# Performance work log

Hardware: AMD Instinct MI355X
Metric: run time of the kernel (lower is better)

Reference implementation:

```python
import jax, jax.numpy as jnp
import numpy as np

HEADS = 8
DIM_HEAD = 64
SCALE = DIM_HEAD ** -0.5


def setup_inputs() -> dict:
    key = jax.random.key(0)
    ks = jax.random.split(key, 5)
    B, N, M, D = 8, 1024, 1024, 512
    inner = HEADS * DIM_HEAD  # 512
    return {
        "x": jax.random.normal(ks[0], (B, N, D), dtype=jnp.float32),
        "context": jax.random.normal(ks[1], (B, M, D), dtype=jnp.float32),
        "Wq": jax.random.normal(ks[2], (D, inner), dtype=jnp.float32) * (D ** -0.5),
        "Wkv": jax.random.normal(ks[3], (D, 2 * inner), dtype=jnp.float32) * (D ** -0.5),
        "Wo": jax.random.normal(ks[4], (inner, D), dtype=jnp.float32) * (inner ** -0.5),
        "bo": jnp.zeros((D,), dtype=jnp.float32),
    }


def reference(x, context, Wq, Wkv, Wo, bo):
    B, N, D = x.shape
    M = context.shape[1]
    q = x @ Wq                      # [B, N, inner]
    kv = context @ Wkv              # [B, M, 2*inner]
    k, v = jnp.split(kv, 2, axis=-1)
    # b n (h d) -> b h n d
    split_heads = lambda t: t.reshape(t.shape[0], t.shape[1], HEADS, DIM_HEAD).transpose(0, 2, 1, 3)
    q, k, v = split_heads(q), split_heads(k), split_heads(v)
    dots = jnp.einsum('bhid,bhjd->bhij', q, k) * SCALE  # [B, H, N, M]
    attn = jax.nn.softmax(dots, axis=-1)
    out = jnp.einsum('bhij,bhjd->bhid', attn, v)        # [B, H, N, d]
    out = out.transpose(0, 2, 1, 3).reshape(B, N, HEADS * DIM_HEAD)
    return out @ Wo + bo            # [B, N, D]
```

## Files before the change

### kernel.cpp

```cpp
#include <hip/hip_runtime.h>
#include <stdint.h>

#define LOG2E 1.44269504088896340736f
#define QSCALE (0.125f * LOG2E)

typedef __bf16 bf16x8 __attribute__((ext_vector_type(8)));
typedef float floatx4 __attribute__((ext_vector_type(4)));

__device__ __forceinline__ unsigned short bfbits(float f) {
  __bf16 h = (__bf16)f;
  return __builtin_bit_cast(unsigned short, h);
}

__device__ __forceinline__ float fast_exp2(float x) {
#if __has_builtin(__builtin_amdgcn_exp2f)
  return __builtin_amdgcn_exp2f(x);
#else
  return exp2f(x);
#endif
}

__device__ __forceinline__ void gl2lds16(const void* g, void* l) {
  __builtin_amdgcn_global_load_lds((const __attribute__((address_space(1))) void*)g,
                                   (__attribute__((address_space(3))) void*)l, 16, 0, 0);
}

__global__ __launch_bounds__(256)
void prep_kernel(const float* __restrict__ x, const float* __restrict__ ctx,
                 const float* __restrict__ Wq, const float* __restrict__ Wkv,
                 const float* __restrict__ Wo,
                 unsigned short* __restrict__ Xb, unsigned short* __restrict__ Cb,
                 unsigned short* __restrict__ WqT, unsigned short* __restrict__ WkvT,
                 unsigned short* __restrict__ WoT) {
  int blk = blockIdx.x;
  int tid = threadIdx.x;
  if (blk < 8192) {
    const float* in = blk < 4096 ? x : ctx;
    unsigned short* out = blk < 4096 ? Xb : Cb;
    int i = (((blk & 4095) * 256) + tid) * 4;
    float4 v = *(const float4*)(in + i);
    unsigned long long pk = (unsigned long long)bfbits(v.x)
                          | ((unsigned long long)bfbits(v.y) << 16)
                          | ((unsigned long long)bfbits(v.z) << 32)
                          | ((unsigned long long)bfbits(v.w) << 48);
    *(unsigned long long*)(out + i) = pk;
  } else {
    __shared__ float tile[32][33];
    int t = blk - 8192;
    const float* in; unsigned short* out; int N; int tb;
    if (t < 256)      { in = Wq;  out = WqT;  N = 512;  tb = t; }
    else if (t < 768) { in = Wkv; out = WkvT; N = 1024; tb = t - 256; }
    else              { in = Wo;  out = WoT;  N = 512;  tb = t - 768; }
    const int K = 512;
    int nbx = N / 32;
    int n0 = (tb % nbx) * 32, k0 = (tb / nbx) * 32;
    int tx = tid & 31, ty = tid >> 5;
#pragma unroll
    for (int r = ty; r < 32; r += 8)
      tile[r][tx] = in[(long)(k0 + r) * N + n0 + tx];
    __syncthreads();
#pragma unroll
    for (int r = ty; r < 32; r += 8)
      out[(long)(n0 + r) * K + k0 + tx] = bfbits(tile[tx][r]);
  }
}

__global__ __launch_bounds__(256)
void proj_gemm(const unsigned short* __restrict__ Xb, const unsigned short* __restrict__ Cb,
               const unsigned short* __restrict__ WqT, const unsigned short* __restrict__ WkvT,
               unsigned short* __restrict__ Qb, unsigned short* __restrict__ Kb,
               unsigned short* __restrict__ Vt) {
  __shared__ unsigned short As[128 * 32];
  __shared__ unsigned short Bs[128 * 32];

  int idx = blockIdx.x;
  const unsigned short* A; const unsigned short* Bt;
  long bm, bn; int role;
  if (idx < 256) { role = 0; A = Xb; Bt = WqT;  bn = (long)(idx & 3) * 128; bm = (long)(idx >> 2) * 128; }
  else { idx -= 256; role = 1; A = Cb; Bt = WkvT; bn = (long)(idx & 7) * 128; bm = (long)(idx >> 3) * 128; }

  const int tid = threadIdx.x;
  const int wave = tid >> 6;
  const int lane = tid & 63;
  const int l15 = lane & 15;
  const int q4 = lane >> 4;
  const int wm = (wave & 1) * 64;
  const int wn = (wave >> 1) * 64;
  const int K = 512;

  floatx4 acc[4][4];
#pragma unroll
  for (int i = 0; i < 4; ++i)
#pragma unroll
    for (int j = 0; j < 4; ++j) { acc[i][j][0]=0.f; acc[i][j][1]=0.f; acc[i][j][2]=0.f; acc[i][j][3]=0.f; }

  for (int k0 = 0; k0 < K; k0 += 32) {
#pragma unroll
    for (int cc = 0; cc < 2; ++cc) {
      int c = cc * 256 + tid;
      int r = c >> 2, kc = c & 3;
      gl2lds16(A + (bm + r) * (long)K + k0 + kc * 8, (char*)As + c * 16);
      gl2lds16(Bt + (bn + r) * (long)K + k0 + kc * 8, (char*)Bs + c * 16);
    }
    __syncthreads();
    bf16x8 af[4], bfr[4];
#pragma unroll
    for (int i = 0; i < 4; ++i)
      af[i] = *(const bf16x8*)(As + (wm + i * 16 + l15) * 32 + q4 * 8);
#pragma unroll
    for (int j = 0; j < 4; ++j)
      bfr[j] = *(const bf16x8*)(Bs + (wn + j * 16 + l15) * 32 + q4 * 8);
#pragma unroll
    for (int i = 0; i < 4; ++i)
#pragma unroll
      for (int j = 0; j < 4; ++j)
        acc[i][j] = __builtin_amdgcn_mfma_f32_16x16x32_bf16(af[i], bfr[j], acc[i][j], 0, 0, 0);
    __syncthreads();
  }

  const bool vrole = (role == 1) && (bn >= 512);
#pragma unroll
  for (int i = 0; i < 4; ++i) {
#pragma unroll
    for (int j = 0; j < 4; ++j) {
      long col = bn + wn + j * 16 + l15;
      if (vrole) {
        long h = (col - 512) >> 6, d = col & 63;
        long row0 = bm + wm + i * 16 + q4 * 4;
        long b = row0 >> 10, m0 = row0 & 1023;
        unsigned long long pk = (unsigned long long)bfbits(acc[i][j][0])
                              | ((unsigned long long)bfbits(acc[i][j][1]) << 16)
                              | ((unsigned long long)bfbits(acc[i][j][2]) << 32)
                              | ((unsigned long long)bfbits(acc[i][j][3]) << 48);
        *(unsigned long long*)(Vt + ((b * 8 + h) * 64 + d) * 1024 + m0) = pk;
      } else {
        long h = col >> 6, d = col & 63;
#pragma unroll
        for (int r = 0; r < 4; ++r) {
          long row = bm + wm + i * 16 + q4 * 4 + r;
          long b = row >> 10, n = row & 1023;
          float v = acc[i][j][r];
          if (role == 0) Qb[((b * 8 + h) * 1024 + n) * 64 + d] = bfbits(v * QSCALE);
          else           Kb[((b * 8 + h) * 1024 + n) * 64 + d] = bfbits(v);
        }
      }
    }
  }
}

__global__ __launch_bounds__(256)
void attn_kernel(const unsigned short* __restrict__ Qb,
                 const unsigned short* __restrict__ Kb,
                 const unsigned short* __restrict__ Vt,
                 unsigned short* __restrict__ Ob)
{
  __shared__ unsigned short Ksm[2][4096];
  __shared__ unsigned short Vsm[2][4096];
  __shared__ unsigned short Psm[64 * 64];

  const int tid = threadIdx.x;
  const int wave = tid >> 6;
  const int lane = tid & 63;
  const int l15 = lane & 15;
  const int q4 = lane >> 4;
  const int bh = blockIdx.x;
  const int nb = blockIdx.y;

  bf16x8 qf[2];
#pragma unroll
  for (int ks = 0; ks < 2; ++ks)
    qf[ks] = *(const bf16x8*)(Qb + ((long)bh * 1024 + nb * 64 + wave * 16 + l15) * 64 + ks * 32 + q4 * 8);

  floatx4 acc[4];
#pragma unroll
  for (int d = 0; d < 4; ++d) { acc[d][0]=0.f; acc[d][1]=0.f; acc[d][2]=0.f; acc[d][3]=0.f; }
  float suml = 0.0f;

  const unsigned short* Kbase = Kb + (long)bh * 65536;
  const unsigned short* Vbase = Vt + (long)bh * 65536;
  int koff[2], voff[2], lds16[2];
#pragma unroll
  for (int cc = 0; cc < 2; ++cc) {
    int c = cc * 256 + tid;
    int jrow = c >> 3;
    int cact = (c & 7) ^ (jrow & 7);
    koff[cc] = jrow * 64 + cact * 8;
    voff[cc] = jrow * 1024 + cact * 8;
    lds16[cc] = c * 16;
  }
#pragma unroll
  for (int cc = 0; cc < 2; ++cc) {
    gl2lds16(Kbase + koff[cc], (char*)Ksm[0] + lds16[cc]);
    gl2lds16(Vbase + voff[cc], (char*)Vsm[0] + lds16[cc]);
  }

  const int prow = wave * 16 + l15;

  for (int t = 0; t < 16; ++t) {
    __syncthreads();
    const int cur = t & 1;
    if (t + 1 < 16) {
      const int nxt = cur ^ 1;
#pragma unroll
      for (int cc = 0; cc < 2; ++cc) {
        gl2lds16(Kbase + (t + 1) * 4096 + koff[cc], (char*)Ksm[nxt] + lds16[cc]);
        gl2lds16(Vbase + (t + 1) * 64 + voff[cc], (char*)Vsm[nxt] + lds16[cc]);
      }
    }

    floatx4 st[4];
#pragma unroll
    for (int jn = 0; jn < 4; ++jn) { st[jn][0]=0.f; st[jn][1]=0.f; st[jn][2]=0.f; st[jn][3]=0.f; }
#pragma unroll
    for (int ks = 0; ks < 2; ++ks) {
      bf16x8 kfr[4];
#pragma unroll
      for (int jn = 0; jn < 4; ++jn) {
        int j = jn * 16 + l15;
        int cact = (ks * 4 + q4) ^ (j & 7);
        kfr[jn] = *(const bf16x8*)(Ksm[cur] + j * 64 + cact * 8);
      }
#pragma unroll
      for (int jn = 0; jn < 4; ++jn)
        st[jn] = __builtin_amdgcn_mfma_f32_16x16x32_bf16(kfr[jn], qf[ks], st[jn], 0, 0, 0);
    }

#pragma unroll
    for (int jn = 0; jn < 4; ++jn) {
      float p0 = fast_exp2(st[jn][0]);
      float p1 = fast_exp2(st[jn][1]);
      float p2 = fast_exp2(st[jn][2]);
      float p3 = fast_exp2(st[jn][3]);
      suml += (p0 + p1) + (p2 + p3);
      unsigned long long pk = (unsigned long long)bfbits(p0)
                            | ((unsigned long long)bfbits(p1) << 16)
                            | ((unsigned long long)bfbits(p2) << 32)
                            | ((unsigned long long)bfbits(p3) << 48);
      int ch8 = (jn * 2 + (q4 >> 1)) ^ (prow & 7);
      *(unsigned long long*)(Psm + prow * 64 + ch8 * 8 + (q4 & 1) * 4) = pk;
    }
    __asm__ volatile("s_waitcnt lgkmcnt(0)" ::: "memory");

#pragma unroll
    for (int ks = 0; ks < 2; ++ks) {
      bf16x8 pa = *(const bf16x8*)(Psm + prow * 64 + (((ks * 4 + q4) ^ (prow & 7)) * 8));
      bf16x8 vb[4];
#pragma unroll
      for (int dn = 0; dn < 4; ++dn) {
        int dd = dn * 16 + l15;
        int cact = (ks * 4 + q4) ^ (dd & 7);
        vb[dn] = *(const bf16x8*)(Vsm[cur] + dd * 64 + cact * 8);
      }
#pragma unroll
      for (int dn = 0; dn < 4; ++dn)
        acc[dn] = __builtin_amdgcn_mfma_f32_16x16x32_bf16(pa, vb[dn], acc[dn], 0, 0, 0);
    }
  }

  float l = suml;
  l += __shfl_xor(l, 16, 64);
  l += __shfl_xor(l, 32, 64);
  float inv = 1.0f / l;
  float invr[4];
#pragma unroll
  for (int r = 0; r < 4; ++r) invr[r] = __shfl(inv, q4 * 4 + r, 64);

  const int b = bh >> 3, h = bh & 7;
#pragma unroll
  for (int dn = 0; dn < 4; ++dn) {
#pragma unroll
    for (int r = 0; r < 4; ++r) {
      long row = (long)b * 1024 + nb * 64 + wave * 16 + q4 * 4 + r;
      long col = h * 64 + dn * 16 + l15;
      Ob[row * 512 + col] = bfbits(acc[dn][r] * invr[r]);
    }
  }
}

__global__ __launch_bounds__(256)
void out_gemm(const unsigned short* __restrict__ A,
              const unsigned short* __restrict__ Bt,
              float* __restrict__ outF, const float* __restrict__ bias) {
  __shared__ unsigned short As[64 * 32];
  __shared__ unsigned short Bs[128 * 32];

  const int tid = threadIdx.x;
  const int wave = tid >> 6;
  const int lane = tid & 63;
  const int l15 = lane & 15;
  const int q4 = lane >> 4;
  const int wm = (wave & 1) * 32;
  const int wn = (wave >> 1) * 64;
  const long bm = (long)blockIdx.y * 64;
  const long bn = (long)blockIdx.x * 128;
  const int K = 512, N = 512;

  floatx4 acc[2][4];
#pragma unroll
  for (int i = 0; i < 2; ++i)
#pragma unroll
    for (int j = 0; j < 4; ++j) { acc[i][j][0]=0.f; acc[i][j][1]=0.f; acc[i][j][2]=0.f; acc[i][j][3]=0.f; }

  for (int k0 = 0; k0 < K; k0 += 32) {
    {
      int r = tid >> 2, kc = tid & 3;
      gl2lds16(A + (bm + r) * (long)K + k0 + kc * 8, (char*)As + tid * 16);
    }
#pragma unroll
    for (int cc = 0; cc < 2; ++cc) {
      int c = cc * 256 + tid;
      int r = c >> 2, kc = c & 3;
      gl2lds16(Bt + (bn + r) * (long)K + k0 + kc * 8, (char*)Bs + c * 16);
    }
    __syncthreads();
    bf16x8 af[2], bfr[4];
#pragma unroll
    for (int i = 0; i < 2; ++i)
      af[i] = *(const bf16x8*)(As + (wm + i * 16 + l15) * 32 + q4 * 8);
#pragma unroll
    for (int j = 0; j < 4; ++j)
      bfr[j] = *(const bf16x8*)(Bs + (wn + j * 16 + l15) * 32 + q4 * 8);
#pragma unroll
    for (int i = 0; i < 2; ++i)
#pragma unroll
      for (int j = 0; j < 4; ++j)
        acc[i][j] = __builtin_amdgcn_mfma_f32_16x16x32_bf16(af[i], bfr[j], acc[i][j], 0, 0, 0);
    __syncthreads();
  }

#pragma unroll
  for (int i = 0; i < 2; ++i) {
#pragma unroll
    for (int j = 0; j < 4; ++j) {
      long col = bn + wn + j * 16 + l15;
      float bv = bias[col];
#pragma unroll
      for (int r = 0; r < 4; ++r) {
        long row = bm + wm + i * 16 + q4 * 4 + r;
        outF[row * (long)N + col] = acc[i][j][r] + bv;
      }
    }
  }
}

extern "C" void kernel_launch(void* const* d_in, const int* in_sizes, int n_in,
                              void* d_out, int out_size, void* d_ws, size_t ws_size,
                              hipStream_t stream) {
  const float* x   = (const float*)d_in[0];
  const float* ctx = (const float*)d_in[1];
  const float* Wq  = (const float*)d_in[2];
  const float* Wkv = (const float*)d_in[3];
  const float* Wo  = (const float*)d_in[4];
  const float* bo  = (const float*)d_in[5];
  float* out = (float*)d_out;

  char* ws = (char*)d_ws;
  unsigned short* Xb   = (unsigned short*)(ws);
  unsigned short* Cb   = (unsigned short*)(ws + (8u  << 20));
  unsigned short* WqT  = (unsigned short*)(ws + (16u << 20));
  unsigned short* WkvT = (unsigned short*)(ws + (17u << 20));
  unsigned short* WoT  = (unsigned short*)(ws + (19u << 20));
  unsigned short* Qb   = (unsigned short*)(ws + (20u << 20));
  unsigned short* Kb   = (unsigned short*)(ws + (28u << 20));
  unsigned short* Vt   = (unsigned short*)(ws + (36u << 20));
  unsigned short* Ob   = (unsigned short*)(ws + (44u << 20));

  prep_kernel<<<9216, 256, 0, stream>>>(x, ctx, Wq, Wkv, Wo, Xb, Cb, WqT, WkvT, WoT);
  proj_gemm<<<768, 256, 0, stream>>>(Xb, Cb, WqT, WkvT, Qb, Kb, Vt);
  attn_kernel<<<dim3(64, 16), 256, 0, stream>>>(Qb, Kb, Vt, Ob);
  out_gemm<<<dim3(4, 128), 256, 0, stream>>>(Ob, WoT, out, bo);
}
```

Measured before the change: 157.2 us.

## Double attention query tile per block to reuse K/V tiles across 128 rows

Each attention block now processes 128 query rows (32 per wave, two 16-row MFMA sub-tiles) instead of 64, halving the grid along the query dimension. Each K/V tile staged in shared memory is reused by twice as many queries, and K fragments loaded from LDS feed two MFMAs, so global and LDS traffic per unit of work drops. The cost is more registers and a larger P buffer in shared memory, which may lower occupancy, and only 512 blocks are launched.

```diff
diff --git a/kernel.cpp b/kernel.cpp
--- a/kernel.cpp
+++ b/kernel.cpp
@@ -156,7 +156,7 @@
 {
   __shared__ unsigned short Ksm[2][4096];
   __shared__ unsigned short Vsm[2][4096];
-  __shared__ unsigned short Psm[64 * 64];
+  __shared__ unsigned short Psm[128 * 64];
 
   const int tid = threadIdx.x;
   const int wave = tid >> 6;
@@ -166,15 +166,21 @@
   const int bh = blockIdx.x;
   const int nb = blockIdx.y;
 
-  bf16x8 qf[2];
-#pragma unroll
-  for (int ks = 0; ks < 2; ++ks)
-    qf[ks] = *(const bf16x8*)(Qb + ((long)bh * 1024 + nb * 64 + wave * 16 + l15) * 64 + ks * 32 + q4 * 8);
-
-  floatx4 acc[4];
-#pragma unroll
-  for (int d = 0; d < 4; ++d) { acc[d][0]=0.f; acc[d][1]=0.f; acc[d][2]=0.f; acc[d][3]=0.f; }
-  float suml = 0.0f;
+  const long qrow0 = (long)bh * 1024 + nb * 128 + wave * 32;
+
+  bf16x8 qf[2][2];
+#pragma unroll
+  for (int qn = 0; qn < 2; ++qn)
+#pragma unroll
+    for (int ks = 0; ks < 2; ++ks)
+      qf[qn][ks] = *(const bf16x8*)(Qb + (qrow0 + qn * 16 + l15) * 64 + ks * 32 + q4 * 8);
+
+  floatx4 acc[2][4];
+#pragma unroll
+  for (int i = 0; i < 2; ++i)
+#pragma unroll
+    for (int d = 0; d < 4; ++d) { acc[i][d][0]=0.f; acc[i][d][1]=0.f; acc[i][d][2]=0.f; acc[i][d][3]=0.f; }
+  float suml[2] = {0.0f, 0.0f};
 
   const unsigned short* Kbase = Kb + (long)bh * 65536;
   const unsigned short* Vbase = Vt + (long)bh * 65536;
@@ -194,8 +200,6 @@
     gl2lds16(Vbase + voff[cc], (char*)Vsm[0] + lds16[cc]);
   }
 
-  const int prow = wave * 16 + l15;
-
   for (int t = 0; t < 16; ++t) {
     __syncthreads();
     const int cur = t & 1;
@@ -208,9 +212,11 @@
       }
     }
 
-    floatx4 st[4];
-#pragma unroll
-    for (int jn = 0; jn < 4; ++jn) { st[jn][0]=0.f; st[jn][1]=0.f; st[jn][2]=0.f; st[jn][3]=0.f; }
+    floatx4 st[4][2];
+#pragma unroll
+    for (int jn = 0; jn < 4; ++jn)
+#pragma unroll
+      for (int qn = 0; qn < 2; ++qn) { st[jn][qn][0]=0.f; st[jn][qn][1]=0.f; st[jn][qn][2]=0.f; st[jn][qn][3]=0.f; }
 #pragma unroll
     for (int ks = 0; ks < 2; ++ks) {
       bf16x8 kfr[4];
@@ -222,29 +228,40 @@
       }
 #pragma unroll
       for (int jn = 0; jn < 4; ++jn)
-        st[jn] = __builtin_amdgcn_mfma_f32_16x16x32_bf16(kfr[jn], qf[ks], st[jn], 0, 0, 0);
-    }
-
-#pragma unroll
-    for (int jn = 0; jn < 4; ++jn) {
-      float p0 = fast_exp2(st[jn][0]);
-      float p1 = fast_exp2(st[jn][1]);
-      float p2 = fast_exp2(st[jn][2]);
-      float p3 = fast_exp2(st[jn][3]);
-      suml += (p0 + p1) + (p2 + p3);
-      unsigned long long pk = (unsigned long long)bfbits(p0)
-                            | ((unsigned long long)bfbits(p1) << 16)
-                            | ((unsigned long long)bfbits(p2) << 32)
-                            | ((unsigned long long)bfbits(p3) << 48);
-      int ch8 = (jn * 2 + (q4 >> 1)) ^ (prow & 7);
-      *(unsigned long long*)(Psm + prow * 64 + ch8 * 8 + (q4 & 1) * 4) = pk;
+#pragma unroll
+        for (int qn = 0; qn < 2; ++qn)
+          st[jn][qn] = __builtin_amdgcn_mfma_f32_16x16x32_bf16(kfr[jn], qf[qn][ks], st[jn][qn], 0, 0, 0);
+    }
+
+#pragma unroll
+    for (int qn = 0; qn < 2; ++qn) {
+      int prow = wave * 32 + qn * 16 + l15;
+#pragma unroll
+      for (int jn = 0; jn < 4; ++jn) {
+        float p0 = fast_exp2(st[jn][qn][0]);
+        float p1 = fast_exp2(st[jn][qn][1]);
+        float p2 = fast_exp2(st[jn][qn][2]);
+        float p3 = fast_exp2(st[jn][qn][3]);
+        suml[qn] += (p0 + p1) + (p2 + p3);
+        unsigned long long pk = (unsigned long long)bfbits(p0)
+                              | ((unsigned long long)bfbits(p1) << 16)
+                              | ((unsigned long long)bfbits(p2) << 32)
+                              | ((unsigned long long)bfbits(p3) << 48);
+        int ch16 = (jn * 2 + (q4 >> 1)) ^ (prow & 7);
+        *(unsigned long long*)(Psm + prow * 64 + ch16 * 8 + (q4 & 1) * 4) = pk;
+      }
     }
     __asm__ volatile("s_waitcnt lgkmcnt(0)" ::: "memory");
 
 #pragma unroll
     for (int ks = 0; ks < 2; ++ks) {
-      bf16x8 pa = *(const bf16x8*)(Psm + prow * 64 + (((ks * 4 + q4) ^ (prow & 7)) * 8));
-      bf16x8 vb[4];
+      bf16x8 pa[2], vb[4];
+#pragma unroll
+      for (int i = 0; i < 2; ++i) {
+        int m = wave * 32 + i * 16 + l15;
+        int cact = (ks * 4 + q4) ^ (m & 7);
+        pa[i] = *(const bf16x8*)(Psm + m * 64 + cact * 8);
+      }
 #pragma unroll
       for (int dn = 0; dn < 4; ++dn) {
         int dd = dn * 16 + l15;
@@ -252,27 +269,35 @@
         vb[dn] = *(const bf16x8*)(Vsm[cur] + dd * 64 + cact * 8);
       }
 #pragma unroll
-      for (int dn = 0; dn < 4; ++dn)
-        acc[dn] = __builtin_amdgcn_mfma_f32_16x16x32_bf16(pa, vb[dn], acc[dn], 0, 0, 0);
-    }
-  }
-
-  float l = suml;
-  l += __shfl_xor(l, 16, 64);
-  l += __shfl_xor(l, 32, 64);
-  float inv = 1.0f / l;
-  float invr[4];
-#pragma unroll
-  for (int r = 0; r < 4; ++r) invr[r] = __shfl(inv, q4 * 4 + r, 64);
+      for (int i = 0; i < 2; ++i)
+#pragma unroll
+        for (int dn = 0; dn < 4; ++dn)
+          acc[i][dn] = __builtin_amdgcn_mfma_f32_16x16x32_bf16(pa[i], vb[dn], acc[i][dn], 0, 0, 0);
+    }
+  }
+
+  float inv[2], invr[2][4];
+#pragma unroll
+  for (int qn = 0; qn < 2; ++qn) {
+    float l = suml[qn];
+    l += __shfl_xor(l, 16, 64);
+    l += __shfl_xor(l, 32, 64);
+    inv[qn] = 1.0f / l;
+#pragma unroll
+    for (int r = 0; r < 4; ++r) invr[qn][r] = __shfl(inv[qn], q4 * 4 + r, 64);
+  }
 
   const int b = bh >> 3, h = bh & 7;
 #pragma unroll
-  for (int dn = 0; dn < 4; ++dn) {
-#pragma unroll
-    for (int r = 0; r < 4; ++r) {
-      long row = (long)b * 1024 + nb * 64 + wave * 16 + q4 * 4 + r;
-      long col = h * 64 + dn * 16 + l15;
-      Ob[row * 512 + col] = bfbits(acc[dn][r] * invr[r]);
+  for (int i = 0; i < 2; ++i) {
+#pragma unroll
+    for (int dn = 0; dn < 4; ++dn) {
+#pragma unroll
+      for (int r = 0; r < 4; ++r) {
+        long row = (long)b * 1024 + nb * 128 + wave * 32 + i * 16 + q4 * 4 + r;
+        long col = h * 64 + dn * 16 + l15;
+        Ob[row * 512 + col] = bfbits(acc[i][dn][r] * invr[i][r]);
+      }
     }
   }
 }
@@ -367,6 +392,6 @@
 
   prep_kernel<<<9216, 256, 0, stream>>>(x, ctx, Wq, Wkv, Wo, Xb, Cb, WqT, WkvT, WoT);
   proj_gemm<<<768, 256, 0, stream>>>(Xb, Cb, WqT, WkvT, Qb, Kb, Vt);
-  attn_kernel<<<dim3(64, 16), 256, 0, stream>>>(Qb, Kb, Vt, Ob);
+  attn_kernel<<<dim3(64, 8), 256, 0, stream>>>(Qb, Kb, Vt, Ob);
   out_gemm<<<dim3(4, 128), 256, 0, stream>>>(Ob, WoT, out, bo);
 }
```

Result: no change. 156.1 us (-0.7%).
